# Optimization experiments

Hardware: AMD Instinct MI355X
Metric: run time of the kernel (lower is better)

Reference implementation:

```python
import jax, jax.numpy as jnp
import numpy as np

V_MIN = -10.0
V_MAX = 10.0
N_ATOMS = 101
LN_EPS = 1e-5

B = 131072
N_OBS = 60
N_ACT = 20
H = 256


def _layer_norm(x, g, b):
    mu = jnp.mean(x, axis=-1, keepdims=True)
    var = jnp.mean(jnp.square(x - mu), axis=-1, keepdims=True)
    return (x - mu) * jax.lax.rsqrt(var + LN_EPS) * g + b


def _mlp(x, W1, b1, g1, be1, W2, b2, g2, be2, W3, b3, g3, be3, W4, b4):
    h = jax.nn.silu(_layer_norm(x @ W1 + b1, g1, be1))
    h = jax.nn.silu(_layer_norm(h @ W2 + b2, g2, be2))
    h = jax.nn.silu(_layer_norm(h @ W3 + b3, g3, be3))
    return h @ W4 + b4  # [B, N_ATOMS] logits


def setup_inputs() -> dict:
    key = jax.random.key(0)
    ks = jax.random.split(key, 10)
    s = 0.05
    return {
        'obs': jax.random.normal(ks[0], (B, N_OBS), jnp.float32),
        'actions': jax.random.normal(ks[1], (B, N_ACT), jnp.float32),
        'rewards': jax.random.normal(ks[2], (B,), jnp.float32),
        'bootstrap': jax.random.uniform(ks[3], (B,), jnp.float32),
        'discount': jax.random.uniform(ks[4], (B,), jnp.float32, 0.95, 0.99),
        'q_support': jnp.linspace(V_MIN, V_MAX, N_ATOMS, dtype=jnp.float32),
        'W1': jax.random.normal(ks[5], (N_OBS + N_ACT, H), jnp.float32) * s,
        'b1': jnp.zeros((H,), jnp.float32),
        'g1': jnp.ones((H,), jnp.float32),
        'be1': jnp.zeros((H,), jnp.float32),
        'W2': jax.random.normal(ks[6], (H, H // 2), jnp.float32) * s,
        'b2': jnp.zeros((H // 2,), jnp.float32),
        'g2': jnp.ones((H // 2,), jnp.float32),
        'be2': jnp.zeros((H // 2,), jnp.float32),
        'W3': jax.random.normal(ks[7], (H // 2, H // 4), jnp.float32) * s,
        'b3': jnp.zeros((H // 4,), jnp.float32),
        'g3': jnp.ones((H // 4,), jnp.float32),
        'be3': jnp.zeros((H // 4,), jnp.float32),
        'W4': jax.random.normal(ks[8], (H // 4, N_ATOMS), jnp.float32) * s,
        'b4': jnp.zeros((N_ATOMS,), jnp.float32),
    }


def reference(obs, actions, rewards, bootstrap, discount, q_support,
              W1, b1, g1, be1, W2, b2, g2, be2, W3, b3, g3, be3, W4, b4):
    batch = rewards.shape[0]
    delta_z = (V_MAX - V_MIN) / (N_ATOMS - 1)
    # Bellman target support: [B, N_ATOMS]
    target_z = rewards[:, None] + bootstrap[:, None] * discount[:, None] * q_support
    target_z = jnp.clip(target_z, V_MIN, V_MAX)
    b = (target_z - V_MIN) / delta_z
    li = jnp.floor(b).astype(jnp.int32)
    ui = jnp.ceil(b).astype(jnp.int32)
    is_int = ui == li
    lower_mask = is_int & (li > 0)
    upper_mask = is_int & (li == 0)
    li = jnp.where(lower_mask, li - 1, li)
    ui = jnp.where(upper_mask, ui + 1, ui)
    lf = li.astype(b.dtype)
    uf = ui.astype(b.dtype)

    x = jnp.concatenate([obs, actions], axis=-1)
    logits = _mlp(x, W1, b1, g1, be1, W2, b2, g2, be2, W3, b3, g3, be3, W4, b4)
    next_dist = jax.nn.softmax(logits, axis=1)

    size = batch * N_ATOMS
    offset = (jnp.arange(batch, dtype=jnp.int32) * N_ATOMS)[:, None]
    l_idx = jnp.clip((li + offset).reshape(-1), 0, size - 1)
    u_idx = jnp.clip((ui + offset).reshape(-1), 0, size - 1)
    lw = (next_dist * (uf - b)).reshape(-1)
    uw = (next_dist * (b - lf)).reshape(-1)
    proj = jnp.zeros((size,), next_dist.dtype).at[l_idx].add(lw).at[u_idx].add(uw)
    return proj.reshape(batch, N_ATOMS)
```

## Files before the change

kernel.cpp:

```cpp
#include <hip/hip_runtime.h>
#include <math.h>

typedef __bf16 bf16x8 __attribute__((ext_vector_type(8)));
typedef float f32x4 __attribute__((ext_vector_type(4)));

__global__ void conv_weights(const float* __restrict__ W1, const float* __restrict__ W2,
                             const float* __restrict__ W3, const float* __restrict__ W4,
                             const float* __restrict__ b1, const float* __restrict__ g1, const float* __restrict__ be1,
                             const float* __restrict__ b2, const float* __restrict__ g2, const float* __restrict__ be2,
                             const float* __restrict__ b3, const float* __restrict__ g3, const float* __restrict__ be3,
                             const float* __restrict__ b4, const float* __restrict__ qsup,
                             __bf16* __restrict__ ws)
{
  if (blockIdx.x == 36) {
    float* Pp = (float*)(ws + 73728);
    const int t = threadIdx.x;
    Pp[t]       = b1[t];
    Pp[256 + t] = g1[t];
    Pp[512 + t] = be1[t];
    if (t < 128) {
      Pp[768 + t]  = b2[t];
      Pp[896 + t]  = g2[t];
      Pp[1024 + t] = be2[t];
      Pp[1344 + t] = (t < 101) ? b4[t]   : 0.f;
      Pp[1472 + t] = (t < 101) ? qsup[t] : 0.f;
    }
    if (t < 64) {
      Pp[1152 + t] = b3[t];
      Pp[1216 + t] = g3[t];
      Pp[1280 + t] = be3[t];
    }
    return;
  }
  const int f = blockIdx.x * 4 + (threadIdx.x >> 6);
  const int lane = threadIdx.x & 63;
  int f0, ntot, Ksrc, Nsrc, off;
  const float* W;
  if (f < 48)       { f0 = f;       ntot = 16; Ksrc = 80;  Nsrc = 256; W = W1; off = 0; }
  else if (f < 112) { f0 = f - 48;  ntot = 8;  Ksrc = 256; Nsrc = 128; W = W2; off = 24576; }
  else if (f < 128) { f0 = f - 112; ntot = 4;  Ksrc = 128; Nsrc = 64;  W = W3; off = 57344; }
  else              { f0 = f - 128; ntot = 8;  Ksrc = 64;  Nsrc = 101; W = W4; off = 65536; }
  const int kt = f0 / ntot, nt = f0 % ntot;
  const int q = lane >> 4, c = lane & 15;
  const int n = nt * 16 + c;
  bf16x8 v;
#pragma unroll
  for (int j = 0; j < 8; ++j) {
    const int k = kt * 32 + q * 8 + j;
    const float x = (k < Ksrc && n < Nsrc) ? W[k * Nsrc + n] : 0.f;
    v[j] = (__bf16)x;
  }
  ((bf16x8*)(ws + off))[f0 * 64 + lane] = v;
}


__global__ __launch_bounds__(256, 2)
void sacq_wave(const float* __restrict__ obs,  const float* __restrict__ act,
               const float* __restrict__ rew,  const float* __restrict__ boot,
               const float* __restrict__ disc, const float* __restrict__ qsup,
               const float* __restrict__ b1, const float* __restrict__ g1, const float* __restrict__ be1,
               const float* __restrict__ b2, const float* __restrict__ g2, const float* __restrict__ be2,
               const float* __restrict__ b3, const float* __restrict__ g3, const float* __restrict__ be3,
               const float* __restrict__ b4,
               const __bf16* __restrict__ ws,
               float* __restrict__ out)
{
  __shared__ float sm[17536];
  const int t = threadIdx.x;
  const int wv = t >> 6, lane = t & 63;
  const int q = lane >> 4, c = lane & 15;
  float* smw = sm + wv * 4384;
  __bf16* h = (__bf16*)smw;
  float* proj = smw + 1152;
  const int row0w = blockIdx.x * 128 + wv * 32;
  const bf16x8* wsf = (const bf16x8*)ws;
  const float* Pp = (const float*)(const void*)(ws + 73728);

  f32x4 acc1[2][16];
  {
    bf16x8 A1[2][3];
#pragma unroll
    for (int rt = 0; rt < 2; ++rt) {
      const float4* ob4 = (const float4*)(obs + (size_t)(row0w + rt * 16 + c) * 60);
      const float4* ac4 = (const float4*)(act + (size_t)(row0w + rt * 16 + c) * 20);
#pragma unroll
      for (int kt = 0; kt < 3; ++kt) {
        const int k0 = kt * 32 + q * 8;
        float v[8];
        if (k0 < 56) {
          const float4 a = ob4[k0 / 4], b = ob4[k0 / 4 + 1];
          v[0]=a.x; v[1]=a.y; v[2]=a.z; v[3]=a.w; v[4]=b.x; v[5]=b.y; v[6]=b.z; v[7]=b.w;
        } else if (k0 == 56) {
          const float4 a = ob4[14], b = ac4[0];
          v[0]=a.x; v[1]=a.y; v[2]=a.z; v[3]=a.w; v[4]=b.x; v[5]=b.y; v[6]=b.z; v[7]=b.w;
        } else if (k0 < 80) {
          const float4 a = ac4[(k0 - 60) / 4], b = ac4[(k0 - 60) / 4 + 1];
          v[0]=a.x; v[1]=a.y; v[2]=a.z; v[3]=a.w; v[4]=b.x; v[5]=b.y; v[6]=b.z; v[7]=b.w;
        } else {
#pragma unroll
          for (int j = 0; j < 8; ++j) v[j] = 0.f;
        }
#pragma unroll
        for (int j = 0; j < 8; ++j) A1[rt][kt][j] = (__bf16)v[j];
      }
    }
#pragma unroll
    for (int nt = 0; nt < 16; ++nt) {
      const float bb = Pp[nt * 16 + c];
      f32x4 vv = {bb, bb, bb, bb};
      acc1[0][nt] = vv;
      acc1[1][nt] = vv;
    }
#pragma unroll
    for (int ch = 0; ch < 4; ++ch) {
      bf16x8 Bb[3][4];
#pragma unroll
      for (int kt = 0; kt < 3; ++kt)
#pragma unroll
        for (int j = 0; j < 4; ++j)
          Bb[kt][j] = wsf[(kt * 16 + ch * 4 + j) * 64 + lane];
#pragma unroll
      for (int kt = 0; kt < 3; ++kt)
#pragma unroll
        for (int j = 0; j < 4; ++j)
#pragma unroll
          for (int rt = 0; rt < 2; ++rt)
            acc1[rt][ch * 4 + j] = __builtin_amdgcn_mfma_f32_16x16x32_bf16(A1[rt][kt], Bb[kt][j], acc1[rt][ch * 4 + j], 0, 0, 0);
    }
#pragma unroll
    for (int rt = 0; rt < 2; ++rt) {
      float s[4] = {0.f,0.f,0.f,0.f}, s2[4] = {0.f,0.f,0.f,0.f};
#pragma unroll
      for (int nt = 0; nt < 16; ++nt)
#pragma unroll
        for (int r = 0; r < 4; ++r) { const float v = acc1[rt][nt][r]; s[r] += v; s2[r] += v * v; }
      float mu[4], rs[4];
#pragma unroll
      for (int r = 0; r < 4; ++r) {
        s[r] += __shfl_xor(s[r], 1); s2[r] += __shfl_xor(s2[r], 1);
        s[r] += __shfl_xor(s[r], 2); s2[r] += __shfl_xor(s2[r], 2);
        s[r] += __shfl_xor(s[r], 4); s2[r] += __shfl_xor(s2[r], 4);
        s[r] += __shfl_xor(s[r], 8); s2[r] += __shfl_xor(s2[r], 8);
        const float m = s[r] * (1.f / 256.f);
        mu[r] = m;
        rs[r] = rsqrtf(s2[r] * (1.f / 256.f) - m * m + 1e-5f);
      }
#pragma unroll
      for (int nt = 0; nt < 16; ++nt) {
        const int col = nt * 16 + c;
        const float gg = Pp[256 + col], bb = Pp[512 + col];
#pragma unroll
        for (int r = 0; r < 4; ++r) {
          float v = (acc1[rt][nt][r] - mu[r]) * rs[r] * gg + bb;
          v = v * __builtin_amdgcn_rcpf(1.f + __expf(-v));
          h[(rt * 16 + 4 * q + r) * 264 + col] = (__bf16)v;
        }
      }
    }
  }

  {
    f32x4 acc2[2][8];
#pragma unroll
    for (int nt = 0; nt < 8; ++nt) {
      const float bb = Pp[768 + nt * 16 + c];
      f32x4 vv = {bb, bb, bb, bb};
      acc2[0][nt] = vv;
      acc2[1][nt] = vv;
    }
    bf16x8 B2[2][8];
#pragma unroll
    for (int nt = 0; nt < 8; ++nt) B2[0][nt] = wsf[3072 + nt * 64 + lane];
#pragma unroll
    for (int kt = 0; kt < 8; ++kt) {
      if (kt + 1 < 8) {
#pragma unroll
        for (int nt = 0; nt < 8; ++nt)
          B2[(kt + 1) & 1][nt] = wsf[3072 + ((kt + 1) * 8 + nt) * 64 + lane];
      }
      bf16x8 A2r[2];
#pragma unroll
      for (int rt = 0; rt < 2; ++rt)
        A2r[rt] = *(const bf16x8*)(h + (rt * 16 + c) * 264 + kt * 32 + q * 8);
#pragma unroll
      for (int nt = 0; nt < 8; ++nt)
#pragma unroll
        for (int rt = 0; rt < 2; ++rt)
          acc2[rt][nt] = __builtin_amdgcn_mfma_f32_16x16x32_bf16(A2r[rt], B2[kt & 1][nt], acc2[rt][nt], 0, 0, 0);
    }
#pragma unroll
    for (int rt = 0; rt < 2; ++rt) {
      float s[4] = {0.f,0.f,0.f,0.f}, s2[4] = {0.f,0.f,0.f,0.f};
#pragma unroll
      for (int nt = 0; nt < 8; ++nt)
#pragma unroll
        for (int r = 0; r < 4; ++r) { const float v = acc2[rt][nt][r]; s[r] += v; s2[r] += v * v; }
      float mu[4], rs[4];
#pragma unroll
      for (int r = 0; r < 4; ++r) {
        s[r] += __shfl_xor(s[r], 1); s2[r] += __shfl_xor(s2[r], 1);
        s[r] += __shfl_xor(s[r], 2); s2[r] += __shfl_xor(s2[r], 2);
        s[r] += __shfl_xor(s[r], 4); s2[r] += __shfl_xor(s2[r], 4);
        s[r] += __shfl_xor(s[r], 8); s2[r] += __shfl_xor(s2[r], 8);
        const float m = s[r] * (1.f / 128.f);
        mu[r] = m;
        rs[r] = rsqrtf(s2[r] * (1.f / 128.f) - m * m + 1e-5f);
      }
#pragma unroll
      for (int nt = 0; nt < 8; ++nt) {
        const int col = nt * 16 + c;
        const float gg = Pp[896 + col], bb = Pp[1024 + col];
#pragma unroll
        for (int r = 0; r < 4; ++r) {
          float v = (acc2[rt][nt][r] - mu[r]) * rs[r] * gg + bb;
          v = v * __builtin_amdgcn_rcpf(1.f + __expf(-v));
          h[(rt * 16 + 4 * q + r) * 136 + col] = (__bf16)v;
        }
      }
    }
  }

  {
    bf16x8 B3[4][4];
#pragma unroll
    for (int kt = 0; kt < 4; ++kt)
#pragma unroll
      for (int nt = 0; nt < 4; ++nt)
        B3[kt][nt] = wsf[7168 + (kt * 4 + nt) * 64 + lane];
    f32x4 acc3[2][4];
#pragma unroll
    for (int nt = 0; nt < 4; ++nt) {
      const float bb = Pp[1152 + nt * 16 + c];
      f32x4 vv = {bb, bb, bb, bb};
      acc3[0][nt] = vv;
      acc3[1][nt] = vv;
    }
#pragma unroll
    for (int kt = 0; kt < 4; ++kt) {
      bf16x8 A3r[2];
#pragma unroll
      for (int rt = 0; rt < 2; ++rt)
        A3r[rt] = *(const bf16x8*)(h + (rt * 16 + c) * 136 + kt * 32 + q * 8);
#pragma unroll
      for (int nt = 0; nt < 4; ++nt)
#pragma unroll
        for (int rt = 0; rt < 2; ++rt)
          acc3[rt][nt] = __builtin_amdgcn_mfma_f32_16x16x32_bf16(A3r[rt], B3[kt][nt], acc3[rt][nt], 0, 0, 0);
    }
#pragma unroll
    for (int rt = 0; rt < 2; ++rt) {
      float s[4] = {0.f,0.f,0.f,0.f}, s2[4] = {0.f,0.f,0.f,0.f};
#pragma unroll
      for (int nt = 0; nt < 4; ++nt)
#pragma unroll
        for (int r = 0; r < 4; ++r) { const float v = acc3[rt][nt][r]; s[r] += v; s2[r] += v * v; }
      float mu[4], rs[4];
#pragma unroll
      for (int r = 0; r < 4; ++r) {
        s[r] += __shfl_xor(s[r], 1); s2[r] += __shfl_xor(s2[r], 1);
        s[r] += __shfl_xor(s[r], 2); s2[r] += __shfl_xor(s2[r], 2);
        s[r] += __shfl_xor(s[r], 4); s2[r] += __shfl_xor(s2[r], 4);
        s[r] += __shfl_xor(s[r], 8); s2[r] += __shfl_xor(s2[r], 8);
        const float m = s[r] * (1.f / 64.f);
        mu[r] = m;
        rs[r] = rsqrtf(s2[r] * (1.f / 64.f) - m * m + 1e-5f);
      }
#pragma unroll
      for (int nt = 0; nt < 4; ++nt) {
        const int col = nt * 16 + c;
        const float gg = Pp[1216 + col], bb = Pp[1280 + col];
#pragma unroll
        for (int r = 0; r < 4; ++r) {
          float v = (acc3[rt][nt][r] - mu[r]) * rs[r] * gg + bb;
          v = v * __builtin_amdgcn_rcpf(1.f + __expf(-v));
          h[(rt * 16 + 4 * q + r) * 72 + col] = (__bf16)v;
        }
      }
    }
  }

  {
    bf16x8 B4[2][7];
#pragma unroll
    for (int kt = 0; kt < 2; ++kt)
#pragma unroll
      for (int nt = 0; nt < 7; ++nt)
        B4[kt][nt] = wsf[8192 + (kt * 8 + nt) * 64 + lane];
    bf16x8 A4f[2][2];
#pragma unroll
    for (int rt = 0; rt < 2; ++rt)
#pragma unroll
      for (int kt = 0; kt < 2; ++kt)
        A4f[rt][kt] = *(const bf16x8*)(h + (rt * 16 + c) * 72 + kt * 32 + q * 8);

    asm volatile("" ::: "memory");
    {
      f32x4 z = {0.f, 0.f, 0.f, 0.f};
      f32x4* p4 = (f32x4*)proj;
      for (int i = lane; i < 808; i += 64) p4[i] = z;
    }

    f32x4 a4[2][7];
#pragma unroll
    for (int nt = 0; nt < 7; ++nt) {
      const float bb = Pp[1344 + nt * 16 + c];
      f32x4 vv = {bb, bb, bb, bb};
      a4[0][nt] = vv;
      a4[1][nt] = vv;
    }
#pragma unroll
    for (int kt = 0; kt < 2; ++kt)
#pragma unroll
      for (int nt = 0; nt < 7; ++nt)
#pragma unroll
        for (int rt = 0; rt < 2; ++rt)
          a4[rt][nt] = __builtin_amdgcn_mfma_f32_16x16x32_bf16(A4f[rt][kt], B4[kt][nt], a4[rt][nt], 0, 0, 0);

#pragma unroll
    for (int rt = 0; rt < 2; ++rt) {
      float mx4[4] = {-3.4e38f, -3.4e38f, -3.4e38f, -3.4e38f};
#pragma unroll
      for (int nt = 0; nt < 7; ++nt) {
        const bool ok = (nt < 6) | (c < 5);
#pragma unroll
        for (int r = 0; r < 4; ++r)
          if (ok) mx4[r] = fmaxf(mx4[r], a4[rt][nt][r]);
      }
#pragma unroll
      for (int r = 0; r < 4; ++r) {
        mx4[r] = fmaxf(mx4[r], __shfl_xor(mx4[r], 1));
        mx4[r] = fmaxf(mx4[r], __shfl_xor(mx4[r], 2));
        mx4[r] = fmaxf(mx4[r], __shfl_xor(mx4[r], 4));
        mx4[r] = fmaxf(mx4[r], __shfl_xor(mx4[r], 8));
      }
      float sm4[4] = {0.f, 0.f, 0.f, 0.f};
#pragma unroll
      for (int nt = 0; nt < 7; ++nt) {
        const bool ok = (nt < 6) | (c < 5);
#pragma unroll
        for (int r = 0; r < 4; ++r) {
          const float e = ok ? __expf(a4[rt][nt][r] - mx4[r]) : 0.f;
          a4[rt][nt][r] = e;
          sm4[r] += e;
        }
      }
      float inv4[4];
#pragma unroll
      for (int r = 0; r < 4; ++r) {
        float s = sm4[r];
        s += __shfl_xor(s, 1);
        s += __shfl_xor(s, 2);
        s += __shfl_xor(s, 4);
        s += __shfl_xor(s, 8);
        inv4[r] = __builtin_amdgcn_rcpf(s);
      }

      const f32x4 rw4 = *(const f32x4*)(rew  + row0w + rt * 16 + 4 * q);
      const f32x4 bo4 = *(const f32x4*)(boot + row0w + rt * 16 + 4 * q);
      const f32x4 di4 = *(const f32x4*)(disc + row0w + rt * 16 + 4 * q);
      float bd[4];
#pragma unroll
      for (int r = 0; r < 4; ++r) bd[r] = bo4[r] * di4[r];

#pragma unroll
      for (int nt = 0; nt < 7; ++nt) {
        const int col = nt * 16 + c;
        if ((nt < 6) | (c < 5)) {
          const float qsv = Pp[1472 + col];
#pragma unroll
          for (int r = 0; r < 4; ++r) {
            const float p = a4[rt][nt][r] * inv4[r];
            float tz = rw4[r] + bd[r] * qsv;
            tz = fminf(fmaxf(tz, -10.f), 10.f);
            const float b_ = (tz + 10.f) * 5.f;
            const float fl = floorf(b_), cl = ceilf(b_);
            int li = (int)fl, ui = (int)cl;
            if (ui == li) { if (li > 0) --li; else ++ui; }
            const int rb = (rt * 16 + 4 * q + r) * 101;
            atomicAdd(&proj[rb + li], p * ((float)ui - b_));
            atomicAdd(&proj[rb + ui], p * (b_ - (float)li));
          }
        }
      }
    }
  }

  {
    const f32x4* p4 = (const f32x4*)proj;
    f32x4* o4 = (f32x4*)(out + (size_t)row0w * 101);
    for (int i = lane; i < 808; i += 64) o4[i] = p4[i];
  }
}

extern "C" void kernel_launch(void* const* d_in, const int* in_sizes, int n_in,
                              void* d_out, int out_size, void* d_ws, size_t ws_size,
                              hipStream_t stream)
{
  const int B = in_sizes[2];
  __bf16* ws = (__bf16*)d_ws;

  conv_weights<<<dim3(37), dim3(256), 0, stream>>>(
      (const float*)d_in[6],  (const float*)d_in[10], (const float*)d_in[14],
      (const float*)d_in[18],
      (const float*)d_in[7],  (const float*)d_in[8],  (const float*)d_in[9],
      (const float*)d_in[11], (const float*)d_in[12], (const float*)d_in[13],
      (const float*)d_in[15], (const float*)d_in[16], (const float*)d_in[17],
      (const float*)d_in[19], (const float*)d_in[5],  ws);

  sacq_wave<<<dim3(B / 128), dim3(256), 0, stream>>>(
      (const float*)d_in[0],  (const float*)d_in[1],  (const float*)d_in[2],
      (const float*)d_in[3],  (const float*)d_in[4],  (const float*)d_in[5],
      (const float*)d_in[7],  (const float*)d_in[8],  (const float*)d_in[9],
      (const float*)d_in[11], (const float*)d_in[12], (const float*)d_in[13],
      (const float*)d_in[15], (const float*)d_in[16], (const float*)d_in[17],
      (const float*)d_in[19], ws, (float*)d_out);
}
```

Baseline: 332.7 us.

## Transpose MFMA operands so each lane owns one row, simplifying reductions

Swaps the MFMA A/B operands so weights act as the row operand and activations as columns. Each lane then holds four consecutive features of a single batch row. LayerNorm and softmax reductions shrink from four per-lane values with four shuffle levels to one value with two shuffles. Parameters load as float4 vectors and activations are written back as packed bf16x4 stores. The projection also reuses one row's reward and discount per lane, and simplifies the floor/ceil bin logic to a clamped floor with lw = p - uw. That simplification relies on the bin edge case being equivalent to the reference.

```diff
diff --git a/kernel.cpp b/kernel.cpp
--- a/kernel.cpp
+++ b/kernel.cpp
@@ -2,6 +2,7 @@
 #include <math.h>
 
 typedef __bf16 bf16x8 __attribute__((ext_vector_type(8)));
+typedef __bf16 bf16x4 __attribute__((ext_vector_type(4)));
 typedef float f32x4 __attribute__((ext_vector_type(4)));
 
 __global__ void conv_weights(const float* __restrict__ W1, const float* __restrict__ W2,
@@ -74,7 +75,8 @@
   float* proj = smw + 1152;
   const int row0w = blockIdx.x * 128 + wv * 32;
   const bf16x8* wsf = (const bf16x8*)ws;
-  const float* Pp = (const float*)(const void*)(ws + 73728);
+  const f32x4* P4 = (const f32x4*)(const void*)(ws + 73728);
+  const int fq = 4 * q;
 
   f32x4 acc1[2][16];
   {
@@ -105,56 +107,50 @@
       }
     }
 #pragma unroll
-    for (int nt = 0; nt < 16; ++nt) {
-      const float bb = Pp[nt * 16 + c];
-      f32x4 vv = {bb, bb, bb, bb};
-      acc1[0][nt] = vv;
-      acc1[1][nt] = vv;
+    for (int mt = 0; mt < 16; ++mt) {
+      const f32x4 pb = P4[4 * mt + q];
+      acc1[0][mt] = pb;
+      acc1[1][mt] = pb;
     }
 #pragma unroll
     for (int ch = 0; ch < 4; ++ch) {
-      bf16x8 Bb[3][4];
+      bf16x8 Wb[3][4];
 #pragma unroll
       for (int kt = 0; kt < 3; ++kt)
 #pragma unroll
         for (int j = 0; j < 4; ++j)
-          Bb[kt][j] = wsf[(kt * 16 + ch * 4 + j) * 64 + lane];
+          Wb[kt][j] = wsf[(kt * 16 + ch * 4 + j) * 64 + lane];
 #pragma unroll
       for (int kt = 0; kt < 3; ++kt)
 #pragma unroll
         for (int j = 0; j < 4; ++j)
 #pragma unroll
           for (int rt = 0; rt < 2; ++rt)
-            acc1[rt][ch * 4 + j] = __builtin_amdgcn_mfma_f32_16x16x32_bf16(A1[rt][kt], Bb[kt][j], acc1[rt][ch * 4 + j], 0, 0, 0);
-    }
-#pragma unroll
-    for (int rt = 0; rt < 2; ++rt) {
-      float s[4] = {0.f,0.f,0.f,0.f}, s2[4] = {0.f,0.f,0.f,0.f};
-#pragma unroll
-      for (int nt = 0; nt < 16; ++nt)
-#pragma unroll
-        for (int r = 0; r < 4; ++r) { const float v = acc1[rt][nt][r]; s[r] += v; s2[r] += v * v; }
-      float mu[4], rs[4];
-#pragma unroll
-      for (int r = 0; r < 4; ++r) {
-        s[r] += __shfl_xor(s[r], 1); s2[r] += __shfl_xor(s2[r], 1);
-        s[r] += __shfl_xor(s[r], 2); s2[r] += __shfl_xor(s2[r], 2);
-        s[r] += __shfl_xor(s[r], 4); s2[r] += __shfl_xor(s2[r], 4);
-        s[r] += __shfl_xor(s[r], 8); s2[r] += __shfl_xor(s2[r], 8);
-        const float m = s[r] * (1.f / 256.f);
-        mu[r] = m;
-        rs[r] = rsqrtf(s2[r] * (1.f / 256.f) - m * m + 1e-5f);
-      }
-#pragma unroll
-      for (int nt = 0; nt < 16; ++nt) {
-        const int col = nt * 16 + c;
-        const float gg = Pp[256 + col], bb = Pp[512 + col];
-#pragma unroll
-        for (int r = 0; r < 4; ++r) {
-          float v = (acc1[rt][nt][r] - mu[r]) * rs[r] * gg + bb;
-          v = v * __builtin_amdgcn_rcpf(1.f + __expf(-v));
-          h[(rt * 16 + 4 * q + r) * 264 + col] = (__bf16)v;
-        }
+            acc1[rt][ch * 4 + j] = __builtin_amdgcn_mfma_f32_16x16x32_bf16(Wb[kt][j], A1[rt][kt], acc1[rt][ch * 4 + j], 0, 0, 0);
+    }
+#pragma unroll
+    for (int rt = 0; rt < 2; ++rt) {
+      float s = 0.f, s2 = 0.f;
+#pragma unroll
+      for (int mt = 0; mt < 16; ++mt)
+#pragma unroll
+        for (int r = 0; r < 4; ++r) { const float v = acc1[rt][mt][r]; s += v; s2 += v * v; }
+      s += __shfl_xor(s, 16); s2 += __shfl_xor(s2, 16);
+      s += __shfl_xor(s, 32); s2 += __shfl_xor(s2, 32);
+      const float mu = s * (1.f / 256.f);
+      const float rs = rsqrtf(s2 * (1.f / 256.f) - mu * mu + 1e-5f);
+#pragma unroll
+      for (int mt = 0; mt < 16; ++mt) {
+        const f32x4 g4  = P4[64 + 4 * mt + q];
+        const f32x4 be4 = P4[128 + 4 * mt + q];
+        bf16x4 o;
+#pragma unroll
+        for (int r = 0; r < 4; ++r) {
+          float x = (acc1[rt][mt][r] - mu) * rs * g4[r] + be4[r];
+          x = x * __builtin_amdgcn_rcpf(1.f + __expf(-x));
+          o[r] = (__bf16)x;
+        }
+        *(bf16x4*)(h + (rt * 16 + c) * 264 + 16 * mt + fq) = o;
       }
     }
   }
@@ -162,78 +158,71 @@
   {
     f32x4 acc2[2][8];
 #pragma unroll
-    for (int nt = 0; nt < 8; ++nt) {
-      const float bb = Pp[768 + nt * 16 + c];
-      f32x4 vv = {bb, bb, bb, bb};
-      acc2[0][nt] = vv;
-      acc2[1][nt] = vv;
-    }
-    bf16x8 B2[2][8];
-#pragma unroll
-    for (int nt = 0; nt < 8; ++nt) B2[0][nt] = wsf[3072 + nt * 64 + lane];
+    for (int mt = 0; mt < 8; ++mt) {
+      const f32x4 pb = P4[192 + 4 * mt + q];
+      acc2[0][mt] = pb;
+      acc2[1][mt] = pb;
+    }
+    bf16x8 W2f[2][8];
+#pragma unroll
+    for (int mt = 0; mt < 8; ++mt) W2f[0][mt] = wsf[3072 + mt * 64 + lane];
 #pragma unroll
     for (int kt = 0; kt < 8; ++kt) {
       if (kt + 1 < 8) {
 #pragma unroll
-        for (int nt = 0; nt < 8; ++nt)
-          B2[(kt + 1) & 1][nt] = wsf[3072 + ((kt + 1) * 8 + nt) * 64 + lane];
+        for (int mt = 0; mt < 8; ++mt)
+          W2f[(kt + 1) & 1][mt] = wsf[3072 + ((kt + 1) * 8 + mt) * 64 + lane];
       }
       bf16x8 A2r[2];
 #pragma unroll
       for (int rt = 0; rt < 2; ++rt)
         A2r[rt] = *(const bf16x8*)(h + (rt * 16 + c) * 264 + kt * 32 + q * 8);
 #pragma unroll
-      for (int nt = 0; nt < 8; ++nt)
+      for (int mt = 0; mt < 8; ++mt)
 #pragma unroll
         for (int rt = 0; rt < 2; ++rt)
-          acc2[rt][nt] = __builtin_amdgcn_mfma_f32_16x16x32_bf16(A2r[rt], B2[kt & 1][nt], acc2[rt][nt], 0, 0, 0);
-    }
-#pragma unroll
-    for (int rt = 0; rt < 2; ++rt) {
-      float s[4] = {0.f,0.f,0.f,0.f}, s2[4] = {0.f,0.f,0.f,0.f};
-#pragma unroll
-      for (int nt = 0; nt < 8; ++nt)
-#pragma unroll
-        for (int r = 0; r < 4; ++r) { const float v = acc2[rt][nt][r]; s[r] += v; s2[r] += v * v; }
-      float mu[4], rs[4];
-#pragma unroll
-      for (int r = 0; r < 4; ++r) {
-        s[r] += __shfl_xor(s[r], 1); s2[r] += __shfl_xor(s2[r], 1);
-        s[r] += __shfl_xor(s[r], 2); s2[r] += __shfl_xor(s2[r], 2);
-        s[r] += __shfl_xor(s[r], 4); s2[r] += __shfl_xor(s2[r], 4);
-        s[r] += __shfl_xor(s[r], 8); s2[r] += __shfl_xor(s2[r], 8);
-        const float m = s[r] * (1.f / 128.f);
-        mu[r] = m;
-        rs[r] = rsqrtf(s2[r] * (1.f / 128.f) - m * m + 1e-5f);
-      }
-#pragma unroll
-      for (int nt = 0; nt < 8; ++nt) {
-        const int col = nt * 16 + c;
-        const float gg = Pp[896 + col], bb = Pp[1024 + col];
-#pragma unroll
-        for (int r = 0; r < 4; ++r) {
-          float v = (acc2[rt][nt][r] - mu[r]) * rs[r] * gg + bb;
-          v = v * __builtin_amdgcn_rcpf(1.f + __expf(-v));
-          h[(rt * 16 + 4 * q + r) * 136 + col] = (__bf16)v;
-        }
-      }
-    }
-  }
-
-  {
-    bf16x8 B3[4][4];
+          acc2[rt][mt] = __builtin_amdgcn_mfma_f32_16x16x32_bf16(W2f[kt & 1][mt], A2r[rt], acc2[rt][mt], 0, 0, 0);
+    }
+#pragma unroll
+    for (int rt = 0; rt < 2; ++rt) {
+      float s = 0.f, s2 = 0.f;
+#pragma unroll
+      for (int mt = 0; mt < 8; ++mt)
+#pragma unroll
+        for (int r = 0; r < 4; ++r) { const float v = acc2[rt][mt][r]; s += v; s2 += v * v; }
+      s += __shfl_xor(s, 16); s2 += __shfl_xor(s2, 16);
+      s += __shfl_xor(s, 32); s2 += __shfl_xor(s2, 32);
+      const float mu = s * (1.f / 128.f);
+      const float rs = rsqrtf(s2 * (1.f / 128.f) - mu * mu + 1e-5f);
+#pragma unroll
+      for (int mt = 0; mt < 8; ++mt) {
+        const f32x4 g4  = P4[224 + 4 * mt + q];
+        const f32x4 be4 = P4[256 + 4 * mt + q];
+        bf16x4 o;
+#pragma unroll
+        for (int r = 0; r < 4; ++r) {
+          float x = (acc2[rt][mt][r] - mu) * rs * g4[r] + be4[r];
+          x = x * __builtin_amdgcn_rcpf(1.f + __expf(-x));
+          o[r] = (__bf16)x;
+        }
+        *(bf16x4*)(h + (rt * 16 + c) * 136 + 16 * mt + fq) = o;
+      }
+    }
+  }
+
+  {
+    bf16x8 W3f[4][4];
 #pragma unroll
     for (int kt = 0; kt < 4; ++kt)
 #pragma unroll
-      for (int nt = 0; nt < 4; ++nt)
-        B3[kt][nt] = wsf[7168 + (kt * 4 + nt) * 64 + lane];
+      for (int mt = 0; mt < 4; ++mt)
+        W3f[kt][mt] = wsf[7168 + (kt * 4 + mt) * 64 + lane];
     f32x4 acc3[2][4];
 #pragma unroll
-    for (int nt = 0; nt < 4; ++nt) {
-      const float bb = Pp[1152 + nt * 16 + c];
-      f32x4 vv = {bb, bb, bb, bb};
-      acc3[0][nt] = vv;
-      acc3[1][nt] = vv;
+    for (int mt = 0; mt < 4; ++mt) {
+      const f32x4 pb = P4[288 + 4 * mt + q];
+      acc3[0][mt] = pb;
+      acc3[1][mt] = pb;
     }
 #pragma unroll
     for (int kt = 0; kt < 4; ++kt) {
@@ -242,50 +231,45 @@
       for (int rt = 0; rt < 2; ++rt)
         A3r[rt] = *(const bf16x8*)(h + (rt * 16 + c) * 136 + kt * 32 + q * 8);
 #pragma unroll
-      for (int nt = 0; nt < 4; ++nt)
+      for (int mt = 0; mt < 4; ++mt)
 #pragma unroll
         for (int rt = 0; rt < 2; ++rt)
-          acc3[rt][nt] = __builtin_amdgcn_mfma_f32_16x16x32_bf16(A3r[rt], B3[kt][nt], acc3[rt][nt], 0, 0, 0);
-    }
-#pragma unroll
-    for (int rt = 0; rt < 2; ++rt) {
-      float s[4] = {0.f,0.f,0.f,0.f}, s2[4] = {0.f,0.f,0.f,0.f};
-#pragma unroll
-      for (int nt = 0; nt < 4; ++nt)
-#pragma unroll
-        for (int r = 0; r < 4; ++r) { const float v = acc3[rt][nt][r]; s[r] += v; s2[r] += v * v; }
-      float mu[4], rs[4];
-#pragma unroll
-      for (int r = 0; r < 4; ++r) {
-        s[r] += __shfl_xor(s[r], 1); s2[r] += __shfl_xor(s2[r], 1);
-        s[r] += __shfl_xor(s[r], 2); s2[r] += __shfl_xor(s2[r], 2);
-        s[r] += __shfl_xor(s[r], 4); s2[r] += __shfl_xor(s2[r], 4);
-        s[r] += __shfl_xor(s[r], 8); s2[r] += __shfl_xor(s2[r], 8);
-        const float m = s[r] * (1.f / 64.f);
-        mu[r] = m;
-        rs[r] = rsqrtf(s2[r] * (1.f / 64.f) - m * m + 1e-5f);
-      }
-#pragma unroll
-      for (int nt = 0; nt < 4; ++nt) {
-        const int col = nt * 16 + c;
-        const float gg = Pp[1216 + col], bb = Pp[1280 + col];
-#pragma unroll
-        for (int r = 0; r < 4; ++r) {
-          float v = (acc3[rt][nt][r] - mu[r]) * rs[r] * gg + bb;
-          v = v * __builtin_amdgcn_rcpf(1.f + __expf(-v));
-          h[(rt * 16 + 4 * q + r) * 72 + col] = (__bf16)v;
-        }
-      }
-    }
-  }
-
-  {
-    bf16x8 B4[2][7];
+          acc3[rt][mt] = __builtin_amdgcn_mfma_f32_16x16x32_bf16(W3f[kt][mt], A3r[rt], acc3[rt][mt], 0, 0, 0);
+    }
+#pragma unroll
+    for (int rt = 0; rt < 2; ++rt) {
+      float s = 0.f, s2 = 0.f;
+#pragma unroll
+      for (int mt = 0; mt < 4; ++mt)
+#pragma unroll
+        for (int r = 0; r < 4; ++r) { const float v = acc3[rt][mt][r]; s += v; s2 += v * v; }
+      s += __shfl_xor(s, 16); s2 += __shfl_xor(s2, 16);
+      s += __shfl_xor(s, 32); s2 += __shfl_xor(s2, 32);
+      const float mu = s * (1.f / 64.f);
+      const float rs = rsqrtf(s2 * (1.f / 64.f) - mu * mu + 1e-5f);
+#pragma unroll
+      for (int mt = 0; mt < 4; ++mt) {
+        const f32x4 g4  = P4[304 + 4 * mt + q];
+        const f32x4 be4 = P4[320 + 4 * mt + q];
+        bf16x4 o;
+#pragma unroll
+        for (int r = 0; r < 4; ++r) {
+          float x = (acc3[rt][mt][r] - mu) * rs * g4[r] + be4[r];
+          x = x * __builtin_amdgcn_rcpf(1.f + __expf(-x));
+          o[r] = (__bf16)x;
+        }
+        *(bf16x4*)(h + (rt * 16 + c) * 72 + 16 * mt + fq) = o;
+      }
+    }
+  }
+
+  {
+    bf16x8 W4f[2][7];
 #pragma unroll
     for (int kt = 0; kt < 2; ++kt)
 #pragma unroll
-      for (int nt = 0; nt < 7; ++nt)
-        B4[kt][nt] = wsf[8192 + (kt * 8 + nt) * 64 + lane];
+      for (int mt = 0; mt < 7; ++mt)
+        W4f[kt][mt] = wsf[8192 + (kt * 8 + mt) * 64 + lane];
     bf16x8 A4f[2][2];
 #pragma unroll
     for (int rt = 0; rt < 2; ++rt)
@@ -302,83 +286,70 @@
 
     f32x4 a4[2][7];
 #pragma unroll
-    for (int nt = 0; nt < 7; ++nt) {
-      const float bb = Pp[1344 + nt * 16 + c];
-      f32x4 vv = {bb, bb, bb, bb};
-      a4[0][nt] = vv;
-      a4[1][nt] = vv;
+    for (int mt = 0; mt < 7; ++mt) {
+      const f32x4 pb = P4[336 + 4 * mt + q];
+      a4[0][mt] = pb;
+      a4[1][mt] = pb;
     }
 #pragma unroll
     for (int kt = 0; kt < 2; ++kt)
 #pragma unroll
-      for (int nt = 0; nt < 7; ++nt)
+      for (int mt = 0; mt < 7; ++mt)
 #pragma unroll
         for (int rt = 0; rt < 2; ++rt)
-          a4[rt][nt] = __builtin_amdgcn_mfma_f32_16x16x32_bf16(A4f[rt][kt], B4[kt][nt], a4[rt][nt], 0, 0, 0);
-
-#pragma unroll
-    for (int rt = 0; rt < 2; ++rt) {
-      float mx4[4] = {-3.4e38f, -3.4e38f, -3.4e38f, -3.4e38f};
-#pragma unroll
-      for (int nt = 0; nt < 7; ++nt) {
-        const bool ok = (nt < 6) | (c < 5);
-#pragma unroll
-        for (int r = 0; r < 4; ++r)
-          if (ok) mx4[r] = fmaxf(mx4[r], a4[rt][nt][r]);
-      }
-#pragma unroll
-      for (int r = 0; r < 4; ++r) {
-        mx4[r] = fmaxf(mx4[r], __shfl_xor(mx4[r], 1));
-        mx4[r] = fmaxf(mx4[r], __shfl_xor(mx4[r], 2));
-        mx4[r] = fmaxf(mx4[r], __shfl_xor(mx4[r], 4));
-        mx4[r] = fmaxf(mx4[r], __shfl_xor(mx4[r], 8));
-      }
-      float sm4[4] = {0.f, 0.f, 0.f, 0.f};
-#pragma unroll
-      for (int nt = 0; nt < 7; ++nt) {
-        const bool ok = (nt < 6) | (c < 5);
-#pragma unroll
-        for (int r = 0; r < 4; ++r) {
-          const float e = ok ? __expf(a4[rt][nt][r] - mx4[r]) : 0.f;
-          a4[rt][nt][r] = e;
-          sm4[r] += e;
-        }
-      }
-      float inv4[4];
-#pragma unroll
-      for (int r = 0; r < 4; ++r) {
-        float s = sm4[r];
-        s += __shfl_xor(s, 1);
-        s += __shfl_xor(s, 2);
-        s += __shfl_xor(s, 4);
-        s += __shfl_xor(s, 8);
-        inv4[r] = __builtin_amdgcn_rcpf(s);
-      }
-
-      const f32x4 rw4 = *(const f32x4*)(rew  + row0w + rt * 16 + 4 * q);
-      const f32x4 bo4 = *(const f32x4*)(boot + row0w + rt * 16 + 4 * q);
-      const f32x4 di4 = *(const f32x4*)(disc + row0w + rt * 16 + 4 * q);
-      float bd[4];
-#pragma unroll
-      for (int r = 0; r < 4; ++r) bd[r] = bo4[r] * di4[r];
-
-#pragma unroll
-      for (int nt = 0; nt < 7; ++nt) {
-        const int col = nt * 16 + c;
-        if ((nt < 6) | (c < 5)) {
-          const float qsv = Pp[1472 + col];
-#pragma unroll
-          for (int r = 0; r < 4; ++r) {
-            const float p = a4[rt][nt][r] * inv4[r];
-            float tz = rw4[r] + bd[r] * qsv;
+          a4[rt][mt] = __builtin_amdgcn_mfma_f32_16x16x32_bf16(W4f[kt][mt], A4f[rt][kt], a4[rt][mt], 0, 0, 0);
+
+#pragma unroll
+    for (int rt = 0; rt < 2; ++rt) {
+      float mx = -3.4e38f;
+#pragma unroll
+      for (int mt = 0; mt < 7; ++mt) {
+#pragma unroll
+        for (int r = 0; r < 4; ++r) {
+          const bool ok = (mt < 6) | (fq + r < 5);
+          if (ok) mx = fmaxf(mx, a4[rt][mt][r]);
+        }
+      }
+      mx = fmaxf(mx, __shfl_xor(mx, 16));
+      mx = fmaxf(mx, __shfl_xor(mx, 32));
+      float sp = 0.f;
+#pragma unroll
+      for (int mt = 0; mt < 7; ++mt) {
+#pragma unroll
+        for (int r = 0; r < 4; ++r) {
+          const bool ok = (mt < 6) | (fq + r < 5);
+          const float e = ok ? __expf(a4[rt][mt][r] - mx) : 0.f;
+          a4[rt][mt][r] = e;
+          sp += e;
+        }
+      }
+      sp += __shfl_xor(sp, 16);
+      sp += __shfl_xor(sp, 32);
+      const float inv = __builtin_amdgcn_rcpf(sp);
+
+      const int gr = row0w + rt * 16 + c;
+      const float rw = rew[gr];
+      const float bd = boot[gr] * disc[gr];
+      const int rb = (rt * 16 + c) * 101;
+
+#pragma unroll
+      for (int mt = 0; mt < 7; ++mt) {
+        const f32x4 qs4 = P4[368 + 4 * mt + q];
+#pragma unroll
+        for (int r = 0; r < 4; ++r) {
+          const bool ok = (mt < 6) | (fq + r < 5);
+          if (ok) {
+            const float p = a4[rt][mt][r] * inv;
+            float tz = rw + bd * qs4[r];
             tz = fminf(fmaxf(tz, -10.f), 10.f);
-            const float b_ = (tz + 10.f) * 5.f;
-            const float fl = floorf(b_), cl = ceilf(b_);
-            int li = (int)fl, ui = (int)cl;
-            if (ui == li) { if (li > 0) --li; else ++ui; }
-            const int rb = (rt * 16 + 4 * q + r) * 101;
-            atomicAdd(&proj[rb + li], p * ((float)ui - b_));
-            atomicAdd(&proj[rb + ui], p * (b_ - (float)li));
+            const float b_ = tz * 5.f + 50.f;
+            const float fl = fminf(floorf(b_), 99.f);
+            const float frac = b_ - fl;
+            const float uw = p * frac;
+            const float lw = p - uw;
+            const int li = (int)fl;
+            atomicAdd(&proj[rb + li], lw);
+            atomicAdd(&proj[rb + li + 1], uw);
           }
         }
       }
```

Measured after the change: 309.7 us. 1.07x faster.
